# Optimization experiments

Hardware: AMD Instinct MI355X
Metric: run time of the kernel (lower is better)

## Reference

```python
import jax, jax.numpy as jnp
import numpy as np

B, N, D_IMG, D_TXT, H, C = 256, 100, 1024, 768, 512, 512
NBLK = 8
EPS = 1e-5


def setup_inputs() -> dict:
    key = jax.random.key(0)
    ks = jax.random.split(key, 24)
    rn = lambda k, s, sc=0.04: jax.random.normal(k, s, jnp.float32) * sc
    return {
        "img_embedding": jax.random.normal(ks[0], (B, D_IMG), jnp.float32),
        "func_text_embedding": jax.random.normal(ks[1], (B, D_TXT), jnp.float32),
        "node_emb": jax.random.normal(ks[2], (B, N, 768), jnp.float32),
        "pos_emb": jax.random.uniform(ks[3], (B, N, 4), jnp.float32),
        # swin head
        "swinbn_g": jnp.ones((D_IMG,)), "swinbn_b": jnp.zeros((D_IMG,)),
        "swinfc_w": rn(ks[4], (H, D_IMG)), "swinfc_b": jnp.zeros((H,)),
        # text head
        "bntext_g": jnp.ones((D_TXT,)), "bntext_b": jnp.zeros((D_TXT,)),
        "fctext_w": rn(ks[5], (H, D_TXT)), "fctext_b": jnp.zeros((H,)),
        # node / bbox heads (BatchNorm1d over channel dim = max_node)
        "bngat_g": jnp.ones((N,)), "bngat_b": jnp.zeros((N,)),
        "fcgat_w": rn(ks[6], (480, 768)), "fcgat_b": jnp.zeros((480,)),
        "bnbbox_g": jnp.ones((N,)), "bnbbox_b": jnp.zeros((N,)),
        "fcbbox_w": rn(ks[7], (32, 4), 0.3), "fcbbox_b": jnp.zeros((32,)),
        # 8 stacked Rs_GCN non-local blocks (1x1 conv weights = [out,in])
        "gcn_theta_w": rn(ks[8], (NBLK, C, C)), "gcn_theta_b": jnp.zeros((NBLK, C)),
        "gcn_phi_w": rn(ks[9], (NBLK, C, C)), "gcn_phi_b": jnp.zeros((NBLK, C)),
        "gcn_g_w": rn(ks[10], (NBLK, C, C)), "gcn_g_b": jnp.zeros((NBLK, C)),
        "gcn_W_w": rn(ks[11], (NBLK, C, C)), "gcn_W_b": jnp.zeros((NBLK, C)),
        "gcn_bn_g": jnp.ones((NBLK, C)), "gcn_bn_b": jnp.zeros((NBLK, C)),
        # final classifier
        "ffbn_g": jnp.ones((3 * H,)), "ffbn_b": jnp.zeros((3 * H,)),
        "ff_w": rn(ks[12], (2, 3 * H)), "ff_b": jnp.zeros((2,)),
    }


def _bn2(x, g, b):  # BatchNorm1d on (B, C), training-mode batch stats
    m = x.mean(0)
    v = x.var(0)
    return (x - m) * jax.lax.rsqrt(v + EPS) * g + b


def _bn_ch(x, g, b):  # BatchNorm1d on (B, C, L), channel axis 1
    m = x.mean((0, 2), keepdims=True)
    v = x.var((0, 2), keepdims=True)
    return (x - m) * jax.lax.rsqrt(v + EPS) * g[None, :, None] + b[None, :, None]


def reference(img_embedding, func_text_embedding, node_emb, pos_emb,
              swinbn_g, swinbn_b, swinfc_w, swinfc_b,
              bntext_g, bntext_b, fctext_w, fctext_b,
              bngat_g, bngat_b, fcgat_w, fcgat_b,
              bnbbox_g, bnbbox_b, fcbbox_w, fcbbox_b,
              gcn_theta_w, gcn_theta_b, gcn_phi_w, gcn_phi_b,
              gcn_g_w, gcn_g_b, gcn_W_w, gcn_W_b, gcn_bn_g, gcn_bn_b,
              ffbn_g, ffbn_b, ff_w, ff_b):
    elu = jax.nn.elu
    # image branch: x = elu(swinfc(swinbn(img)))
    x = elu(_bn2(img_embedding, swinbn_g, swinbn_b) @ swinfc_w.T + swinfc_b)
    # text branch: elu(fc_text(bn_text(text)))
    ft = elu(_bn2(func_text_embedding, bntext_g, bntext_b) @ fctext_w.T + fctext_b)
    # node / bbox branches (BN over node dim, then linear over feature dim)
    h = elu(_bn_ch(node_emb, bngat_g, bngat_b) @ fcgat_w.T + fcgat_b)       # (B,N,480)
    p = elu(_bn_ch(pos_emb, bnbbox_g, bnbbox_b) @ fcbbox_w.T + fcbbox_b)    # (B,N,32)
    v = jnp.concatenate([h, p], axis=2).transpose(0, 2, 1)                  # (B,512,N)

    # 8 non-local Rs_GCN blocks
    for i in range(NBLK):
        g_v = jnp.einsum('oc,bcn->bno', gcn_g_w[i], v) + gcn_g_b[i]          # (B,N,C)
        th_v = jnp.einsum('oc,bcn->bno', gcn_theta_w[i], v) + gcn_theta_b[i]  # (B,N,C)
        ph_v = jnp.einsum('oc,bcn->bon', gcn_phi_w[i], v) + gcn_phi_b[i][:, None]  # (B,C,N)
        R = jnp.einsum('bnc,bcm->bnm', th_v, ph_v)                            # (B,N,N)
        A = jax.nn.softmax(R, axis=-1)
        y = jnp.einsum('bnm,bmc->bcn', A, g_v)                                # (B,C,N)
        Wy = jnp.einsum('oc,bcn->bon', gcn_W_w[i], y) + gcn_W_b[i][:, None]
        Wy = _bn_ch(Wy, gcn_bn_g[i], gcn_bn_b[i])
        v = Wy + v                                                            # residual

    emb = v.transpose(0, 2, 1)  # (B,N,512)
    # l2norm normalizes over dim=1 (the node dim), matching the torch code
    emb = emb / jnp.sqrt(jnp.sum(emb * emb, axis=1, keepdims=True))
    h_feature = emb.mean(axis=1)  # (B,512)

    all_feats = jnp.concatenate([x, h_feature, ft], axis=1)  # (B,1536)
    out = _bn2(all_feats, ffbn_g, ffbn_b) @ ff_w.T + ff_b    # (B,2)
    return out
```

## Files before the change

kernel.cpp:

```cpp
#include <hip/hip_runtime.h>
#include <cstddef>

#define EPS 1e-5f

constexpr int Bsz = 256;
constexpr int Nn  = 100;
constexpr int Cc  = 512;
constexpr int BN_ROWS = Bsz * Nn;

__device__ __forceinline__ void gload_lds16(const void* g, void* l) {
    __builtin_amdgcn_global_load_lds(
        (const __attribute__((address_space(1))) void*)g,
        (__attribute__((address_space(3))) void*)l, 16, 0, 0);
}

__global__ void colstats_kernel(const float* __restrict__ x, int M, int Ccols,
                                const float* __restrict__ g, const float* __restrict__ bb,
                                float* __restrict__ s, float* __restrict__ t) {
    int c = blockIdx.x;
    int r = threadIdx.x;
    float v = (r < M) ? x[(size_t)r * Ccols + c] : 0.f;
    __shared__ float ssum[256], ssq[256];
    ssum[r] = v; ssq[r] = v * v;
    __syncthreads();
    for (int off = 128; off > 0; off >>= 1) {
        if (r < off) { ssum[r] += ssum[r + off]; ssq[r] += ssq[r + off]; }
        __syncthreads();
    }
    if (r == 0) {
        float m   = ssum[0] / M;
        float var = ssq[0] / M - m * m;
        float sc  = g[c] * rsqrtf(var + EPS);
        s[c] = sc;
        t[c] = bb[c] - m * sc;
    }
}

__global__ void chstats_kernel(const float* __restrict__ x, int D,
                               const float* __restrict__ g, const float* __restrict__ bb,
                               float* __restrict__ s, float* __restrict__ t) {
    int n = blockIdx.x;
    int tid = threadIdx.x;
    int total = Bsz * D;
    float sum = 0.f, sq = 0.f;
    for (int idx = tid; idx < total; idx += blockDim.x) {
        int b = idx / D, d = idx - b * D;
        float v = x[((size_t)b * Nn + n) * D + d];
        sum += v; sq += v * v;
    }
    __shared__ float ssum[256], ssq[256];
    ssum[tid] = sum; ssq[tid] = sq;
    __syncthreads();
    for (int off = 128; off > 0; off >>= 1) {
        if (tid < off) { ssum[tid] += ssum[tid + off]; ssq[tid] += ssq[tid + off]; }
        __syncthreads();
    }
    if (tid == 0) {
        float m   = ssum[0] / total;
        float var = ssq[0] / total - m * m;
        float sc  = g[n] * rsqrtf(var + EPS);
        s[n] = sc;
        t[n] = bb[n] - m * sc;
    }
}

__global__ void chstats_part_kernel(const float* __restrict__ x, float* __restrict__ npart) {
    int n = blockIdx.x, chunk = blockIdx.y;
    int tid = threadIdx.x;
    float sum = 0.f, sq = 0.f;
    for (int i = tid; i < 3072; i += 256) {
        int rrow = i / 192;
        int q = i - rrow * 192;
        float4 f = *(const float4*)(x + ((size_t)(chunk * 16 + rrow) * Nn + n) * 768 + q * 4);
        sum += f.x + f.y + f.z + f.w;
        sq  += f.x * f.x + f.y * f.y + f.z * f.z + f.w * f.w;
    }
    __shared__ float ss[256], s2[256];
    ss[tid] = sum; s2[tid] = sq;
    __syncthreads();
    for (int off = 128; off > 0; off >>= 1) {
        if (tid < off) { ss[tid] += ss[tid + off]; s2[tid] += s2[tid + off]; }
        __syncthreads();
    }
    if (tid == 0) {
        npart[chunk * 200 + n] = ss[0];
        npart[chunk * 200 + 100 + n] = s2[0];
    }
}

__global__ void chstats_fin_kernel(const float* __restrict__ npart,
                                   const float* __restrict__ g, const float* __restrict__ bb,
                                   float* __restrict__ s, float* __restrict__ t) {
    int n = threadIdx.x;
    if (n >= 100) return;
    float sum = 0.f, sq = 0.f;
    for (int c = 0; c < 16; c++) {
        sum += npart[c * 200 + n];
        sq  += npart[c * 200 + 100 + n];
    }
    const float total = 256.f * 768.f;
    float m   = sum / total;
    float var = sq / total - m * m;
    float sc  = g[n] * rsqrtf(var + EPS);
    s[n] = sc;
    t[n] = bb[n] - m * sc;
}

template <int NORM, bool ELU, bool TB, int KS>
__global__ __launch_bounds__(256) void gemm128_kernel(
    const float* __restrict__ A, const float* __restrict__ B0,
    const float* __restrict__ B1, int nsplit,
    const float* __restrict__ bias,
    const float* __restrict__ s, const float* __restrict__ t,
    int M, int N, int K, int lda, int ldb, int mod,
    float* __restrict__ C, int ldc, int c_off) {
    constexpr int BS = TB ? 132 : 128;
    __shared__ float As[KS * 132];
    __shared__ float Bs[KS * BS];

    int by = blockIdx.x;
    int bm = blockIdx.y * 128;
    const float* B = (by < nsplit) ? B0 : B1;
    int bn = (by < nsplit ? by : by - nsplit) * 128;
    int outcol0 = c_off + by * 128;

    int tid = threadIdx.x;
    int lane = tid & 63, wave = tid >> 6;
    int tx = tid & 15, ty = tid >> 4;

    float acc[8][8] = {};

    for (int k0 = 0; k0 < K; k0 += KS) {
#pragma unroll
        for (int i = 0; i < KS / 8; i++) {
            int id = tid + i * 256;
            int row = id / (KS / 4), q = id % (KS / 4);
            int gr = bm + row;
            float4 f = *(const float4*)(A + (size_t)gr * lda + k0 + q * 4);
            if constexpr (NORM == 2) {
                int n_ = gr % mod; float sc = s[n_], sh = t[n_];
                f.x = f.x * sc + sh; f.y = f.y * sc + sh;
                f.z = f.z * sc + sh; f.w = f.w * sc + sh;
            }
            As[(q * 4 + 0) * 132 + row] = f.x;
            As[(q * 4 + 1) * 132 + row] = f.y;
            As[(q * 4 + 2) * 132 + row] = f.z;
            As[(q * 4 + 3) * 132 + row] = f.w;
        }
        if constexpr (TB) {
#pragma unroll
            for (int i = 0; i < KS / 8; i++) {
                int id = tid + i * 256;
                int row = id / (KS / 4), q = id % (KS / 4);
                int gn = bn + row;
                float4 f = make_float4(0.f, 0.f, 0.f, 0.f);
                if (gn < N) f = *(const float4*)(B + (size_t)gn * ldb + k0 + q * 4);
                Bs[(q * 4 + 0) * BS + row] = f.x;
                Bs[(q * 4 + 1) * BS + row] = f.y;
                Bs[(q * 4 + 2) * BS + row] = f.z;
                Bs[(q * 4 + 3) * BS + row] = f.w;
            }
        } else {
#pragma unroll
            for (int i = 0; i < KS / 8; i++) {
                int r = i * 8 + wave * 2 + (lane >> 5);
                gload_lds16(B + (size_t)(k0 + r) * ldb + bn + (lane & 31) * 4,
                            (char*)&Bs[r * BS]);
            }
        }
        __syncthreads();
#pragma unroll 16
        for (int kk = 0; kk < KS; kk++) {
            float4 a0 = *(const float4*)&As[kk * 132 + ty * 4];
            float4 a1 = *(const float4*)&As[kk * 132 + ty * 4 + 64];
            float4 b0 = *(const float4*)&Bs[kk * BS + tx * 4];
            float4 b1 = *(const float4*)&Bs[kk * BS + tx * 4 + 64];
            float av[8] = {a0.x, a0.y, a0.z, a0.w, a1.x, a1.y, a1.z, a1.w};
            float bv[8] = {b0.x, b0.y, b0.z, b0.w, b1.x, b1.y, b1.z, b1.w};
#pragma unroll
            for (int i = 0; i < 8; i++)
#pragma unroll
                for (int j = 0; j < 8; j++)
                    acc[i][j] = fmaf(av[i], bv[j], acc[i][j]);
        }
        __syncthreads();
    }

#pragma unroll
    for (int i = 0; i < 8; i++) {
        int r = ty * 4 + (i & 3) + ((i & 4) ? 64 : 0);
        int gr = bm + r;
        if (gr >= M) continue;
        float* crow = C + (size_t)gr * ldc + outcol0;
#pragma unroll
        for (int h = 0; h < 2; h++) {
            int cl = tx * 4 + h * 64;
            int gcol = bn + cl;
            if constexpr (TB) { if (gcol >= N) continue; }
            float4 o;
            o.x = acc[i][h * 4 + 0]; o.y = acc[i][h * 4 + 1];
            o.z = acc[i][h * 4 + 2]; o.w = acc[i][h * 4 + 3];
            if (bias) {
                o.x += bias[gcol]; o.y += bias[gcol + 1];
                o.z += bias[gcol + 2]; o.w += bias[gcol + 3];
            }
            if constexpr (ELU) {
                o.x = o.x > 0.f ? o.x : expm1f(o.x);
                o.y = o.y > 0.f ? o.y : expm1f(o.y);
                o.z = o.z > 0.f ? o.z : expm1f(o.z);
                o.w = o.w > 0.f ? o.w : expm1f(o.w);
            }
            *(float4*)(crow + cl) = o;
        }
    }
}

template <int NORM, bool ELU, bool TB>
__global__ void gemm_kernel(const float* __restrict__ A, const float* __restrict__ B,
                            const float* __restrict__ bias,
                            const float* __restrict__ s, const float* __restrict__ t,
                            int M, int N, int K, int lda, int ldb, int mod,
                            float* __restrict__ Cout, int ldc, int c_off) {
    __shared__ float As[16][65];
    __shared__ float Bs[16][65];

    int bm = blockIdx.x * 64, bn = blockIdx.y * 64;
    int tid = threadIdx.x;
    int tm = (tid >> 4) << 2;
    int tn = (tid & 15) << 2;
    float acc[4][4] = {};

    for (int k0 = 0; k0 < K; k0 += 16) {
#pragma unroll
        for (int i = 0; i < 4; i++) {
            int idx = tid + i * 256;
            {
                int rr = idx >> 4, kk = idx & 15;
                int gr = bm + rr, gk = k0 + kk;
                float av = 0.f;
                if (gr < M && gk < K) {
                    av = A[(size_t)gr * lda + gk];
                    if constexpr (NORM == 1) av = av * s[gk] + t[gk];
                    else if constexpr (NORM == 2) { int n_ = gr % mod; av = av * s[n_] + t[n_]; }
                }
                As[kk][rr] = av;
            }
            if constexpr (TB) {
                int nn = idx >> 4, kk = idx & 15;
                int gn = bn + nn, gk = k0 + kk;
                Bs[kk][nn] = (gn < N && gk < K) ? B[(size_t)gn * ldb + gk] : 0.f;
            } else {
                int kk = idx >> 6, nn = idx & 63;
                int gn = bn + nn, gk = k0 + kk;
                Bs[kk][nn] = (gn < N && gk < K) ? B[(size_t)gk * ldb + gn] : 0.f;
            }
        }
        __syncthreads();
#pragma unroll
        for (int kk = 0; kk < 16; kk++) {
            float a0[4], b0[4];
#pragma unroll
            for (int i = 0; i < 4; i++) a0[i] = As[kk][tm + i];
#pragma unroll
            for (int j = 0; j < 4; j++) b0[j] = Bs[kk][tn + j];
#pragma unroll
            for (int i = 0; i < 4; i++)
#pragma unroll
                for (int j = 0; j < 4; j++)
                    acc[i][j] = fmaf(a0[i], b0[j], acc[i][j]);
        }
        __syncthreads();
    }

#pragma unroll
    for (int i = 0; i < 4; i++) {
        int gr = bm + tm + i;
        if (gr >= M) continue;
#pragma unroll
        for (int j = 0; j < 4; j++) {
            int gn = bn + tn + j;
            if (gn >= N) continue;
            float v = acc[i][j] + (bias ? bias[gn] : 0.f);
            if constexpr (ELU) v = v > 0.f ? v : expm1f(v);
            Cout[(size_t)gr * ldc + c_off + gn] = v;
        }
    }
}

__global__ __launch_bounds__(256) void compose_kernel(
    const float* __restrict__ th, const float* __restrict__ ph,
    const float* __restrict__ g, const float* __restrict__ W,
    float* __restrict__ Mw, float* __restrict__ WGT) {
    __shared__ float As[32][33];
    __shared__ float Bs[32][68];
    int z = blockIdx.z;
    const float* A = z ? g : th;
    int bm = blockIdx.x * 32, bn = blockIdx.y * 64;
    int tid = threadIdx.x;
    int tm = (tid >> 4) * 2, tn = (tid & 15) * 4;
    float acc[2][4] = {};

    for (int k0 = 0; k0 < Cc; k0 += 32) {
#pragma unroll
        for (int i = 0; i < 4; i++) {
            int id = tid + i * 256;
            int kk = id >> 5, m = id & 31;
            As[kk][m] = A[(size_t)(k0 + kk) * Cc + bm + m];
        }
#pragma unroll
        for (int i = 0; i < 8; i++) {
            int id = tid + i * 256;
            if (z == 0) {
                int kk = id >> 6, n = id & 63;
                Bs[kk][n] = ph[(size_t)(k0 + kk) * Cc + bn + n];
            } else {
                int n = id >> 5, kk = id & 31;
                Bs[kk][n] = W[(size_t)(bn + n) * Cc + k0 + kk];
            }
        }
        __syncthreads();
#pragma unroll
        for (int kk = 0; kk < 32; kk++) {
            float a0 = As[kk][tm], a1 = As[kk][tm + 1];
            float4 b4 = *(const float4*)&Bs[kk][tn];
            acc[0][0] = fmaf(a0, b4.x, acc[0][0]);
            acc[0][1] = fmaf(a0, b4.y, acc[0][1]);
            acc[0][2] = fmaf(a0, b4.z, acc[0][2]);
            acc[0][3] = fmaf(a0, b4.w, acc[0][3]);
            acc[1][0] = fmaf(a1, b4.x, acc[1][0]);
            acc[1][1] = fmaf(a1, b4.y, acc[1][1]);
            acc[1][2] = fmaf(a1, b4.z, acc[1][2]);
            acc[1][3] = fmaf(a1, b4.w, acc[1][3]);
        }
        __syncthreads();
    }
    float* out = z ? WGT : Mw;
    *(float4*)&out[(size_t)(bm + tm) * Cc + bn + tn] =
        make_float4(acc[0][0], acc[0][1], acc[0][2], acc[0][3]);
    *(float4*)&out[(size_t)(bm + tm + 1) * Cc + bn + tn] =
        make_float4(acc[1][0], acc[1][1], acc[1][2], acc[1][3]);
}

__global__ void bbox_kernel(const float* __restrict__ pos, const float* __restrict__ w,
                            const float* __restrict__ bias, const float* __restrict__ s,
                            const float* __restrict__ t, float* __restrict__ V) {
    __shared__ float ws[32][4];
    int tid = threadIdx.x;
    if (tid < 128) ws[tid >> 2][tid & 3] = w[tid];
    __syncthreads();
    int r = blockIdx.x * 8 + (tid >> 5);
    int o = tid & 31;
    int n = r % Nn;
    float sc = s[n], sh = t[n];
    float p0 = pos[(size_t)r * 4 + 0] * sc + sh;
    float p1 = pos[(size_t)r * 4 + 1] * sc + sh;
    float p2 = pos[(size_t)r * 4 + 2] * sc + sh;
    float p3 = pos[(size_t)r * 4 + 3] * sc + sh;
    float acc = bias[o] + p0 * ws[o][0] + p1 * ws[o][1] + p2 * ws[o][2] + p3 * ws[o][3];
    acc = acc > 0.f ? acc : expm1f(acc);
    V[(size_t)r * Cc + 480 + o] = acc;
}

__global__ void q2_kernel(const float* __restrict__ phi, const float* __restrict__ thb,
                          float* __restrict__ q2) {
    int c = blockIdx.x;
    int l = threadIdx.x;
    float acc = 0.f;
    for (int j = l; j < Cc; j += 64) acc += phi[(size_t)j * Cc + c] * thb[j];
    for (int off = 32; off > 0; off >>= 1) acc += __shfl_xor(acc, off, 64);
    if (l == 0) q2[c] = acc;
}
__global__ void cconst_kernel(const float* __restrict__ W, const float* __restrict__ gb,
                              const float* __restrict__ Wb, float* __restrict__ cc) {
    int o = blockIdx.x;
    int l = threadIdx.x;
    float acc = 0.f;
    for (int j = l; j < Cc; j += 64) acc += W[(size_t)o * Cc + j] * gb[j];
    for (int off = 32; off > 0; off >>= 1) acc += __shfl_xor(acc, off, 64);
    if (l == 0) cc[o] = acc + Wb[o];
}
__global__ void colterm_kernel(const float* __restrict__ V, const float* __restrict__ q2,
                               float* __restrict__ ct) {
    int r = blockIdx.x * 4 + (threadIdx.x >> 6);
    int l = threadIdx.x & 63;
    const float* p = V + (size_t)r * Cc;
    float acc = 0.f;
    for (int c = l; c < Cc; c += 64) acc += p[c] * q2[c];
    for (int off = 32; off > 0; off >>= 1) acc += __shfl_xor(acc, off, 64);
    if (l == 0) ct[r] = acc;
}

__global__ __launch_bounds__(256) void attn_rs_kernel(
    const float* __restrict__ TZ, const float* __restrict__ V,
    const float* __restrict__ ct, float* __restrict__ Abuf) {
    __shared__ float smem[5400];
    float* Ts = smem;
    float* Vs = smem + 1800;
    float* A_lds = smem;

    int b = blockIdx.y;
    int rh = blockIdx.x;
    int row0 = b * Nn + rh * 50;
    int tid = threadIdx.x;
    int tx = tid & 31, ty = tid >> 5;

    float acc[7][4];
#pragma unroll
    for (int i = 0; i < 7; i++)
#pragma unroll
        for (int j = 0; j < 4; j++) acc[i][j] = 0.f;

    for (int kt = 0; kt < 16; kt++) {
        __syncthreads();
        for (int i = tid; i < 1200; i += 256) {
            if (i < 400) {
                int r = i >> 3, q = i & 7;
                float4 f = *(const float4*)(TZ + (size_t)(row0 + r) * 1024 + kt * 32 + q * 4);
                *(float4*)&Ts[r * 36 + q * 4] = f;
            } else {
                int ii = i - 400;
                int r = ii >> 3, q = ii & 7;
                float4 f = *(const float4*)(V + (size_t)(b * Nn + r) * 512 + kt * 32 + q * 4);
                *(float4*)&Vs[r * 36 + q * 4] = f;
            }
        }
        __syncthreads();
#pragma unroll
        for (int q = 0; q < 8; q++) {
            float4 av[7];
#pragma unroll
            for (int i = 0; i < 7; i++)
                av[i] = *(const float4*)&Ts[(ty * 7 + i) * 36 + q * 4];
            float4 bv[4];
#pragma unroll
            for (int j = 0; j < 4; j++)
                bv[j] = *(const float4*)&Vs[(tx + 32 * j) * 36 + q * 4];
#pragma unroll
            for (int kk = 0; kk < 4; kk++) {
#pragma unroll
                for (int i = 0; i < 7; i++) {
                    float a = ((const float*)&av[i])[kk];
#pragma unroll
                    for (int j = 0; j < 4; j++)
                        acc[i][j] = fmaf(a, ((const float*)&bv[j])[kk], acc[i][j]);
                }
            }
        }
    }
    __syncthreads();

    float ctv[4];
#pragma unroll
    for (int j = 0; j < 4; j++) {
        int c = tx + 32 * j;
        ctv[j] = (c < Nn) ? ct[b * Nn + c] : 0.f;
    }
#pragma unroll
    for (int i = 0; i < 7; i++) {
        int r = ty * 7 + i;
        if (r >= 50) continue;
#pragma unroll
        for (int j = 0; j < 4; j++) {
            int c = tx + 32 * j;
            if (c < Nn) A_lds[r * 105 + c] = acc[i][j] + ctv[j];
        }
    }
    __syncthreads();
    if (tid < 50) {
        float* row = A_lds + tid * 105;
        float mx = -1e30f;
        for (int m = 0; m < Nn; m++) mx = fmaxf(mx, row[m]);
        float sm = 0.f;
        for (int m = 0; m < Nn; m++) { float e = expf(row[m] - mx); row[m] = e; sm += e; }
        float inv = 1.f / sm;
        for (int m = 0; m < Nn; m++) row[m] *= inv;
    }
    __syncthreads();
    for (int i = tid; i < 5000; i += 256) {
        int r = i / 100, c = i - r * 100;
        Abuf[(size_t)(row0 + r) * 104 + c] = A_lds[r * 105 + c];
    }
}

__global__ __launch_bounds__(256) void pv_kernel(
    float* __restrict__ TZ, const float* __restrict__ Abuf,
    const float* __restrict__ cc, float* __restrict__ part) {
    __shared__ float Zs[25 * 256];
    __shared__ float As2[50 * 28];
    int b  = blockIdx.z;
    int rh = blockIdx.x;
    int ch = blockIdx.y;
    int row0 = b * Nn + rh * 50;
    int tid = threadIdx.x;
    int lane = tid & 63, wave = tid >> 6;
    int tx = tid & 31, ty = tid >> 5;

    float acc[7][8];
#pragma unroll
    for (int i = 0; i < 7; i++)
#pragma unroll
        for (int j = 0; j < 8; j++) acc[i][j] = 0.f;

    for (int kt = 0; kt < 4; kt++) {
        __syncthreads();
        for (int r = wave; r < 25; r += 4) {
            gload_lds16(TZ + (size_t)(b * Nn + kt * 25 + r) * 1024 + 512 + ch * 256 + lane * 4,
                        (char*)&Zs[r * 256]);
        }
        for (int i = tid; i < 1250; i += 256) {
            int r = i / 25, k = i - r * 25;
            As2[r * 28 + k] = Abuf[(size_t)(row0 + r) * 104 + kt * 25 + k];
        }
        __syncthreads();
#pragma unroll 5
        for (int k = 0; k < 25; k++) {
            float av[7];
#pragma unroll
            for (int i = 0; i < 7; i++) av[i] = As2[(ty * 7 + i) * 28 + k];
            float zv[8];
#pragma unroll
            for (int j = 0; j < 8; j++) zv[j] = Zs[k * 256 + tx + 32 * j];
#pragma unroll
            for (int i = 0; i < 7; i++)
#pragma unroll
                for (int j = 0; j < 8; j++)
                    acc[i][j] = fmaf(av[i], zv[j], acc[i][j]);
        }
    }

    float ccv[8];
#pragma unroll
    for (int j = 0; j < 8; j++) ccv[j] = cc[ch * 256 + tx + 32 * j];
    float psum[8], psq[8];
#pragma unroll
    for (int j = 0; j < 8; j++) { psum[j] = 0.f; psq[j] = 0.f; }
#pragma unroll
    for (int i = 0; i < 7; i++) {
        int r = ty * 7 + i;
        if (r >= 50) continue;
        float* orow = TZ + (size_t)(row0 + r) * 1024 + ch * 256;
#pragma unroll
        for (int j = 0; j < 8; j++) {
            float v = acc[i][j] + ccv[j];
            orow[tx + 32 * j] = v;
            psum[j] += v; psq[j] += v * v;
        }
    }
    __syncthreads();
    float* sums = Zs;
#pragma unroll
    for (int j = 0; j < 8; j++) {
        int c = tx + 32 * j;
        sums[ty * 512 + c] = psum[j];
        sums[ty * 512 + 256 + c] = psq[j];
    }
    __syncthreads();
    {
        float ssv = 0.f, sqv = 0.f;
        for (int y = 0; y < 8; y++) {
            ssv += sums[y * 512 + tid & 0 ? 0 : y * 512 + tid];
        }
        ssv = 0.f; sqv = 0.f;
        for (int y = 0; y < 8; y++) {
            ssv += sums[y * 512 + tid];
            sqv += sums[y * 512 + 256 + tid];
        }
        int pair = b * 2 + rh;
        if (tid < 256) {
            part[(size_t)pair * 1024 + ch * 256 + tid] = ssv;
            part[(size_t)pair * 1024 + 512 + ch * 256 + tid] = sqv;
        }
    }
}

__global__ void wy_fin2_kernel(const float* __restrict__ part,
                               const float* __restrict__ g, const float* __restrict__ bb,
                               float* __restrict__ s, float* __restrict__ t) {
    int c = blockIdx.x;
    int l = threadIdx.x;
    float sum = 0.f, sq = 0.f;
    for (int p = l; p < 512; p += 64) {
        sum += part[(size_t)p * 1024 + c];
        sq  += part[(size_t)p * 1024 + 512 + c];
    }
    for (int off = 32; off > 0; off >>= 1) {
        sum += __shfl_xor(sum, off, 64);
        sq  += __shfl_xor(sq, off, 64);
    }
    if (l == 0) {
        float m   = sum / BN_ROWS;
        float var = sq / BN_ROWS - m * m;
        float sc  = g[c] * rsqrtf(var + EPS);
        s[c] = sc;
        t[c] = bb[c] - m * sc;
    }
}

__global__ void residual_kernel(float* __restrict__ V, const float* __restrict__ Wy, int ldw,
                                const float* __restrict__ s, const float* __restrict__ t) {
    size_t total4 = (size_t)BN_ROWS * Cc / 4;
    for (size_t i4 = (size_t)blockIdx.x * blockDim.x + threadIdx.x; i4 < total4;
         i4 += (size_t)gridDim.x * blockDim.x) {
        int row = (int)(i4 >> 7);
        int c = (int)(i4 & 127) * 4;
        float4 w = *(const float4*)(Wy + (size_t)row * ldw + c);
        float4 sv = *(const float4*)(s + c);
        float4 tv = *(const float4*)(t + c);
        float4 v = *(float4*)(V + (size_t)row * Cc + c);
        v.x += w.x * sv.x + tv.x; v.y += w.y * sv.y + tv.y;
        v.z += w.z * sv.z + tv.z; v.w += w.w * sv.w + tv.w;
        *(float4*)(V + (size_t)row * Cc + c) = v;
    }
}

__global__ void l2norm_mean_kernel(const float* __restrict__ V, float* __restrict__ ALL) {
    int b = blockIdx.x;
    int c = threadIdx.x;
    float sum = 0.f, sq = 0.f;
    const float* p = V + (size_t)b * Nn * Cc + c;
    for (int n = 0; n < Nn; n++) {
        float v = p[(size_t)n * Cc];
        sum += v; sq += v * v;
    }
    ALL[(size_t)b * 1536 + 512 + c] = sum / (Nn * sqrtf(sq));
}

__global__ void final_kernel(const float* __restrict__ ALL, const float* __restrict__ s,
                             const float* __restrict__ t, const float* __restrict__ w,
                             const float* __restrict__ bias, float* __restrict__ out) {
    int b = blockIdx.x;
    int tid = threadIdx.x;
    float p0 = 0.f, p1 = 0.f;
    for (int k = tid; k < 1536; k += 256) {
        float af = ALL[(size_t)b * 1536 + k] * s[k] + t[k];
        p0 += af * w[k];
        p1 += af * w[1536 + k];
    }
    __shared__ float s0[256], s1[256];
    s0[tid] = p0; s1[tid] = p1;
    __syncthreads();
    for (int off = 128; off > 0; off >>= 1) {
        if (tid < off) { s0[tid] += s0[tid + off]; s1[tid] += s1[tid + off]; }
        __syncthreads();
    }
    if (tid == 0) {
        out[b * 2 + 0] = s0[0] + bias[0];
        out[b * 2 + 1] = s1[0] + bias[1];
    }
}

extern "C" void kernel_launch(void* const* d_in, const int* in_sizes, int n_in,
                              void* d_out, int out_size, void* d_ws, size_t ws_size,
                              hipStream_t stream) {
    const float* img   = (const float*)d_in[0];
    const float* txt   = (const float*)d_in[1];
    const float* node  = (const float*)d_in[2];
    const float* pos   = (const float*)d_in[3];
    const float* swinbn_g = (const float*)d_in[4];
    const float* swinbn_b = (const float*)d_in[5];
    const float* swinfc_w = (const float*)d_in[6];
    const float* swinfc_b = (const float*)d_in[7];
    const float* bntext_g = (const float*)d_in[8];
    const float* bntext_b = (const float*)d_in[9];
    const float* fctext_w = (const float*)d_in[10];
    const float* fctext_b = (const float*)d_in[11];
    const float* bngat_g  = (const float*)d_in[12];
    const float* bngat_b  = (const float*)d_in[13];
    const float* fcgat_w  = (const float*)d_in[14];
    const float* fcgat_b  = (const float*)d_in[15];
    const float* bnbbox_g = (const float*)d_in[16];
    const float* bnbbox_b = (const float*)d_in[17];
    const float* fcbbox_w = (const float*)d_in[18];
    const float* fcbbox_b = (const float*)d_in[19];
    const float* gcn_theta_w = (const float*)d_in[20];
    const float* gcn_theta_b = (const float*)d_in[21];
    const float* gcn_phi_w   = (const float*)d_in[22];
    const float* gcn_phi_b   = (const float*)d_in[23];
    const float* gcn_g_w     = (const float*)d_in[24];
    const float* gcn_g_b     = (const float*)d_in[25];
    const float* gcn_W_w     = (const float*)d_in[26];
    const float* gcn_W_b     = (const float*)d_in[27];
    const float* gcn_bn_g    = (const float*)d_in[28];
    const float* gcn_bn_b    = (const float*)d_in[29];
    const float* ffbn_g = (const float*)d_in[30];
    const float* ffbn_b = (const float*)d_in[31];
    const float* ff_w   = (const float*)d_in[32];
    const float* ff_b   = (const float*)d_in[33];

    float* ws = (float*)d_ws;
    const size_t VN = (size_t)BN_ROWS * Cc;
    float* V    = ws;
    float* TZ   = V + VN;
    float* Abuf = TZ + VN * 2;
    float* Mw   = Abuf + (size_t)BN_ROWS * 104;
    float* WGT  = Mw + (size_t)Cc * Cc;
    float* ALL  = WGT + (size_t)Cc * Cc;
    float* ct   = ALL + (size_t)Bsz * 1536;
    float* part = ct + BN_ROWS;
    float* st   = part + 524288;
    float* s_img = st;            float* t_img = s_img + 1024;
    float* s_txt = t_img + 1024;  float* t_txt = s_txt + 768;
    float* s_nd  = t_txt + 768;   float* t_nd  = s_nd + 128;
    float* s_bb  = t_nd + 128;    float* t_bb  = s_bb + 128;
    float* s_g   = t_bb + 128;    float* t_g   = s_g + 512;
    float* s_ff  = t_g + 512;     float* t_ff  = s_ff + 1536;
    float* q2    = t_ff + 1536;   float* cc    = q2 + 512;

    dim3 blk(256);

    colstats_kernel<<<1024, 256, 0, stream>>>(img, 256, 1024, swinbn_g, swinbn_b, s_img, t_img);
    colstats_kernel<<<768, 256, 0, stream>>>(txt, 256, 768, bntext_g, bntext_b, s_txt, t_txt);
    chstats_part_kernel<<<dim3(100, 16, 1), 256, 0, stream>>>(node, part);
    chstats_fin_kernel<<<1, 128, 0, stream>>>(part, bngat_g, bngat_b, s_nd, t_nd);
    chstats_kernel<<<100, 256, 0, stream>>>(pos, 4, bnbbox_g, bnbbox_b, s_bb, t_bb);

    gemm_kernel<1, true, true><<<dim3(4, 8, 1), blk, 0, stream>>>(
        img, swinfc_w, swinfc_b, s_img, t_img, 256, 512, 1024, 1024, 1024, 0,
        ALL, 1536, 0);
    gemm_kernel<1, true, true><<<dim3(4, 8, 1), blk, 0, stream>>>(
        txt, fctext_w, fctext_b, s_txt, t_txt, 256, 512, 768, 768, 768, 0,
        ALL, 1536, 1024);
    gemm128_kernel<2, true, true, 16><<<dim3(4, 200, 1), blk, 0, stream>>>(
        node, fcgat_w, nullptr, 1 << 30, fcgat_b, s_nd, t_nd,
        25600, 480, 768, 768, 768, 100, V, 512, 0);
    bbox_kernel<<<3200, 256, 0, stream>>>(pos, fcbbox_w, fcbbox_b, s_bb, t_bb, V);

    for (int i = 0; i < 8; i++) {
        const float* thw = gcn_theta_w + (size_t)i * Cc * Cc;
        const float* thb = gcn_theta_b + (size_t)i * Cc;
        const float* phw = gcn_phi_w + (size_t)i * Cc * Cc;
        const float* gw  = gcn_g_w + (size_t)i * Cc * Cc;
        const float* gb  = gcn_g_b + (size_t)i * Cc;
        const float* Ww  = gcn_W_w + (size_t)i * Cc * Cc;
        const float* Wb  = gcn_W_b + (size_t)i * Cc;

        compose_kernel<<<dim3(16, 8, 2), blk, 0, stream>>>(thw, phw, gw, Ww, Mw, WGT);
        q2_kernel<<<512, 64, 0, stream>>>(phw, thb, q2);
        cconst_kernel<<<512, 64, 0, stream>>>(Ww, gb, Wb, cc);
        colterm_kernel<<<6400, 256, 0, stream>>>(V, q2, ct);

        gemm128_kernel<0, false, false, 32><<<dim3(8, 200, 1), blk, 0, stream>>>(
            V, Mw, WGT, 4, nullptr, nullptr, nullptr,
            25600, 1024, 512, 512, 512, 0, TZ, 1024, 0);

        attn_rs_kernel<<<dim3(2, 256, 1), blk, 0, stream>>>(TZ, V, ct, Abuf);
        pv_kernel<<<dim3(2, 2, 256), blk, 0, stream>>>(TZ, Abuf, cc, part);

        wy_fin2_kernel<<<512, 64, 0, stream>>>(part, gcn_bn_g + (size_t)i * Cc,
                                               gcn_bn_b + (size_t)i * Cc, s_g, t_g);
        residual_kernel<<<2048, 256, 0, stream>>>(V, TZ, 1024, s_g, t_g);
    }

    l2norm_mean_kernel<<<256, 512, 0, stream>>>(V, ALL);
    colstats_kernel<<<1536, 256, 0, stream>>>(ALL, 256, 1536, ffbn_g, ffbn_b, s_ff, t_ff);
    final_kernel<<<256, 256, 0, stream>>>(ALL, s_ff, t_ff, ff_w, ff_b, (float*)d_out);
}
```

Baseline: 5.277 ms.

## Remap block IDs for XCD-local L2 reuse and fuse column term into attention

Flattens the grids of the GEMM, attention and PV kernels and remaps block IDs so that consecutive blocks on the same XCD (bid&7) share a contiguous range of batch rows. This is meant to raise L2 hit rates on MI355X's chiplet-partitioned caches. It also removes the separate colterm kernel by computing the V·q2 dot products inside attn_rs_kernel into LDS, saving a launch and a global round trip. The fcgat GEMM moves from K-step 16 to 32, and some dead code in pv_kernel is cleaned up. The remap assumes grid sizes divide evenly by 8 times the column-tile count.

New measurement: 5.204 ms. Within noise of the previous version (-1.4%).

```diff
diff --git a/kernel.cpp b/kernel.cpp
--- a/kernel.cpp
+++ b/kernel.cpp
@@ -106,7 +106,7 @@
     t[n] = bb[n] - m * sc;
 }
 
-template <int NORM, bool ELU, bool TB, int KS>
+template <int NORM, bool ELU, bool TB, int KS, int BYSHIFT>
 __global__ __launch_bounds__(256) void gemm128_kernel(
     const float* __restrict__ A, const float* __restrict__ B0,
     const float* __restrict__ B1, int nsplit,
@@ -118,8 +118,14 @@
     __shared__ float As[KS * 132];
     __shared__ float Bs[KS * BS];
 
-    int by = blockIdx.x;
-    int bm = blockIdx.y * 128;
+    int bid = blockIdx.x;
+    int xcd = bid & 7;
+    int l = bid >> 3;
+    int by = l & ((1 << BYSHIFT) - 1);
+    int bmi = l >> BYSHIFT;
+    int bm_per_xcd = (int)(gridDim.x >> (3 + BYSHIFT));
+    int bm = (xcd * bm_per_xcd + bmi) * 128;
+
     const float* B = (by < nsplit) ? B0 : B1;
     int bn = (by < nsplit ? by : by - nsplit) * 128;
     int outcol0 = c_off + by * 128;
@@ -379,30 +385,39 @@
     for (int off = 32; off > 0; off >>= 1) acc += __shfl_xor(acc, off, 64);
     if (l == 0) cc[o] = acc + Wb[o];
 }
-__global__ void colterm_kernel(const float* __restrict__ V, const float* __restrict__ q2,
-                               float* __restrict__ ct) {
-    int r = blockIdx.x * 4 + (threadIdx.x >> 6);
-    int l = threadIdx.x & 63;
-    const float* p = V + (size_t)r * Cc;
-    float acc = 0.f;
-    for (int c = l; c < Cc; c += 64) acc += p[c] * q2[c];
-    for (int off = 32; off > 0; off >>= 1) acc += __shfl_xor(acc, off, 64);
-    if (l == 0) ct[r] = acc;
-}
 
 __global__ __launch_bounds__(256) void attn_rs_kernel(
     const float* __restrict__ TZ, const float* __restrict__ V,
-    const float* __restrict__ ct, float* __restrict__ Abuf) {
-    __shared__ float smem[5400];
+    const float* __restrict__ q2, float* __restrict__ Abuf) {
+    __shared__ float smem[5500];
     float* Ts = smem;
     float* Vs = smem + 1800;
     float* A_lds = smem;
-
-    int b = blockIdx.y;
-    int rh = blockIdx.x;
+    float* ct_lds = smem + 5400;
+
+    int bid = blockIdx.x;
+    int xcd = bid & 7;
+    int l = bid >> 3;
+    int b = xcd * 32 + (l >> 1);
+    int rh = l & 1;
     int row0 = b * Nn + rh * 50;
     int tid = threadIdx.x;
     int tx = tid & 31, ty = tid >> 5;
+
+    {
+        int r = tid >> 1, h = tid & 1;
+        float cacc = 0.f;
+        if (r < Nn) {
+            const float4* vp = (const float4*)(V + (size_t)(b * Nn + r) * 512);
+            const float4* qp = (const float4*)q2;
+            for (int c4 = h; c4 < 128; c4 += 2) {
+                float4 f = vp[c4], q = qp[c4];
+                cacc += f.x * q.x + f.y * q.y + f.z * q.z + f.w * q.w;
+            }
+        }
+        cacc += __shfl_xor(cacc, 1, 64);
+        if (r < Nn && h == 0) ct_lds[r] = cacc;
+    }
 
     float acc[7][4];
 #pragma unroll
@@ -453,7 +468,7 @@
 #pragma unroll
     for (int j = 0; j < 4; j++) {
         int c = tx + 32 * j;
-        ctv[j] = (c < Nn) ? ct[b * Nn + c] : 0.f;
+        ctv[j] = (c < Nn) ? ct_lds[c] : 0.f;
     }
 #pragma unroll
     for (int i = 0; i < 7; i++) {
@@ -487,9 +502,13 @@
     const float* __restrict__ cc, float* __restrict__ part) {
     __shared__ float Zs[25 * 256];
     __shared__ float As2[50 * 28];
-    int b  = blockIdx.z;
-    int rh = blockIdx.x;
-    int ch = blockIdx.y;
+    int bid = blockIdx.x;
+    int xcd = bid & 7;
+    int l = bid >> 3;
+    int b = xcd * 32 + (l >> 2);
+    int sub = l & 3;
+    int rh = sub & 1;
+    int ch = sub >> 1;
     int row0 = b * Nn + rh * 50;
     int tid = threadIdx.x;
     int lane = tid & 63, wave = tid >> 6;
@@ -558,18 +577,12 @@
     {
         float ssv = 0.f, sqv = 0.f;
         for (int y = 0; y < 8; y++) {
-            ssv += sums[y * 512 + tid & 0 ? 0 : y * 512 + tid];
-        }
-        ssv = 0.f; sqv = 0.f;
-        for (int y = 0; y < 8; y++) {
             ssv += sums[y * 512 + tid];
             sqv += sums[y * 512 + 256 + tid];
         }
         int pair = b * 2 + rh;
-        if (tid < 256) {
-            part[(size_t)pair * 1024 + ch * 256 + tid] = ssv;
-            part[(size_t)pair * 1024 + 512 + ch * 256 + tid] = sqv;
-        }
+        part[(size_t)pair * 1024 + ch * 256 + tid] = ssv;
+        part[(size_t)pair * 1024 + 512 + ch * 256 + tid] = sqv;
     }
 }
 
@@ -695,8 +708,7 @@
     float* Mw   = Abuf + (size_t)BN_ROWS * 104;
     float* WGT  = Mw + (size_t)Cc * Cc;
     float* ALL  = WGT + (size_t)Cc * Cc;
-    float* ct   = ALL + (size_t)Bsz * 1536;
-    float* part = ct + BN_ROWS;
+    float* part = ALL + (size_t)Bsz * 1536;
     float* st   = part + 524288;
     float* s_img = st;            float* t_img = s_img + 1024;
     float* s_txt = t_img + 1024;  float* t_txt = s_txt + 768;
@@ -720,7 +732,7 @@
     gemm_kernel<1, true, true><<<dim3(4, 8, 1), blk, 0, stream>>>(
         txt, fctext_w, fctext_b, s_txt, t_txt, 256, 512, 768, 768, 768, 0,
         ALL, 1536, 1024);
-    gemm128_kernel<2, true, true, 16><<<dim3(4, 200, 1), blk, 0, stream>>>(
+    gemm128_kernel<2, true, true, 32, 2><<<800, blk, 0, stream>>>(
         node, fcgat_w, nullptr, 1 << 30, fcgat_b, s_nd, t_nd,
         25600, 480, 768, 768, 768, 100, V, 512, 0);
     bbox_kernel<<<3200, 256, 0, stream>>>(pos, fcbbox_w, fcbbox_b, s_bb, t_bb, V);
@@ -737,14 +749,13 @@
         compose_kernel<<<dim3(16, 8, 2), blk, 0, stream>>>(thw, phw, gw, Ww, Mw, WGT);
         q2_kernel<<<512, 64, 0, stream>>>(phw, thb, q2);
         cconst_kernel<<<512, 64, 0, stream>>>(Ww, gb, Wb, cc);
-        colterm_kernel<<<6400, 256, 0, stream>>>(V, q2, ct);
-
-        gemm128_kernel<0, false, false, 32><<<dim3(8, 200, 1), blk, 0, stream>>>(
+
+        gemm128_kernel<0, false, false, 32, 3><<<1600, blk, 0, stream>>>(
             V, Mw, WGT, 4, nullptr, nullptr, nullptr,
             25600, 1024, 512, 512, 512, 0, TZ, 1024, 0);
 
-        attn_rs_kernel<<<dim3(2, 256, 1), blk, 0, stream>>>(TZ, V, ct, Abuf);
-        pv_kernel<<<dim3(2, 2, 256), blk, 0, stream>>>(TZ, Abuf, cc, part);
+        attn_rs_kernel<<<512, blk, 0, stream>>>(TZ, V, q2, Abuf);
+        pv_kernel<<<1024, blk, 0, stream>>>(TZ, Abuf, cc, part);
 
         wy_fin2_kernel<<<512, 64, 0, stream>>>(part, gcn_bn_g + (size_t)i * Cc,
                                                gcn_bn_b + (size_t)i * Cc, s_g, t_g);
```
